# Performance work log

Hardware: AMD Instinct MI355X
Metric: run time of the kernel (lower is better)

Reference implementation:

```python
import jax, jax.numpy as jnp
import numpy as np
from jax import lax

B = 32768
N_INP = 256
N_HIDDEN = 1024
N_F = 256
N_ITERS = 100  # fixed-point solver iteration count in Convex


def _make_operators(n_f):
    # D = tridiag(-1, 2, -1) with first/last rows zeroed; mid = 0.5 * (sub+super diag ones)
    D = (-np.diag(np.ones(n_f - 1), -1) + 2 * np.diag(np.ones(n_f))
         - np.diag(np.ones(n_f - 1), 1)).astype(np.float32)
    D[0, :] = 0.0
    D[n_f - 1, :] = 0.0
    mid = 0.5 * (np.diag(np.ones(n_f - 1), -1) + np.diag(np.ones(n_f - 1), 1)).astype(np.float32)
    return jnp.asarray(D), jnp.asarray(mid)


def _convex(param):
    # param: [B, n_f]  (the torch code carries [B, n_f, 1]; column vec is equivalent)
    D, mid = _make_operators(param.shape[-1])

    def body(z, _):
        zx = z + param                       # [B, n_f]
        Dz = jnp.einsum('ij,bj->bi', D, zx)  # D @ zx
        mz = jnp.einsum('ij,bj->bi', mid, zx)
        dx = jnp.where(Dz > 0, zx - mz, 0.0)
        return zx - dx - param, None

    z0 = jnp.zeros_like(param)
    z_star, _ = lax.scan(body, z0, None, length=N_ITERS)
    return param + z_star  # Convex.forward: x + model(x)


def setup_inputs() -> dict:
    key = jax.random.key(0)
    k = jax.random.split(key, 5)
    x = jax.random.uniform(k[0], (B, N_INP + 1), dtype=jnp.float32)
    W1 = jax.random.normal(k[1], (N_HIDDEN, N_INP), dtype=jnp.float32) * 0.02
    b1 = jax.random.normal(k[2], (N_HIDDEN,), dtype=jnp.float32) * 0.02
    W2 = jax.random.normal(k[3], (N_F, N_HIDDEN), dtype=jnp.float32) * 0.02
    b2 = jax.random.normal(k[4], (N_F,), dtype=jnp.float32) * 0.02
    return {"x": x, "W1": W1, "b1": b1, "W2": W2, "b2": b2}


def reference(x, W1, b1, W2, b2):
    h = jax.nn.relu(x[..., :N_INP] @ W1.T + b1)     # [B, n_hidden]
    x_ = h @ W2.T + b2                              # [B, n_f]
    param = _convex(x_)                             # [B, n_f]
    # EvalConvex: round(query * (n_f - 1)) -> gather along feature dim
    idx = jnp.round(x[..., N_INP] * (N_F - 1)).astype(jnp.int32)  # [B]
    out = jnp.take_along_axis(param, idx[:, None], axis=1)        # [B, 1]
    return out.reshape(-1, 1, 1)                                  # [B, 1, 1]
```

## Files before the change

### kernel.cpp

```cpp
#include <hip/hip_runtime.h>
#include <stdint.h>

#define B_ROWS 32768
#define N_INP 256
#define N_HID 1024
#define NF 256
#define N_IT 100

typedef __attribute__((ext_vector_type(8))) _Float16 f16x8;
typedef __attribute__((ext_vector_type(4))) float f32x4;
typedef __attribute__((ext_vector_type(2))) _Float16 f16x2;
typedef uint32_t u32;

__device__ __forceinline__ ushort f2h(float f) {
  _Float16 h = (_Float16)f;
  return *reinterpret_cast<ushort*>(&h);
}

__device__ __forceinline__ void async_copy16(const void* g, void* l) {
  __builtin_amdgcn_global_load_lds(
      (const __attribute__((address_space(1))) void*)g,
      (__attribute__((address_space(3))) void*)l, 16, 0, 0);
}

__device__ __forceinline__ f16x2 as_h2(u32 x) { return __builtin_bit_cast(f16x2, x); }
__device__ __forceinline__ u32 as_u32(f16x2 x) { return __builtin_bit_cast(u32, x); }
__device__ __forceinline__ f16x2 min2(f16x2 a, f16x2 b) {
  f16x2 r;
  asm("v_pk_min_f16 %0, %1, %2" : "=v"(r) : "v"(a), "v"(b));
  return r;
}

__global__ void prep_kernel(const float* __restrict__ x,
                            const float* __restrict__ W1,
                            const float* __restrict__ W2,
                            ushort* __restrict__ xh,
                            ushort* __restrict__ w1h,
                            ushort* __restrict__ w2h,
                            int* __restrict__ idx) {
  if (blockIdx.x < 8192) {
    int t = blockIdx.x * 256 + threadIdx.x;
    int b = t >> 6, q = t & 63;
    const float* xr = x + (size_t)b * (N_INP + 1);
    float v0 = xr[q * 4 + 0], v1 = xr[q * 4 + 1], v2 = xr[q * 4 + 2], v3 = xr[q * 4 + 3];
    ushort4 u = make_ushort4(f2h(v0), f2h(v1), f2h(v2), f2h(v3));
    *reinterpret_cast<ushort4*>(xh + (size_t)b * 256 + q * 4) = u;
    if (q == 0) idx[b] = (int)rintf(xr[N_INP] * 255.0f);
  } else {
    int t = (blockIdx.x - 8192) * 256 + threadIdx.x;
    float4 a = reinterpret_cast<const float4*>(W1)[t];
    float4 b = reinterpret_cast<const float4*>(W2)[t];
    reinterpret_cast<ushort4*>(w1h)[t] = make_ushort4(f2h(a.x), f2h(a.y), f2h(a.z), f2h(a.w));
    reinterpret_cast<ushort4*>(w2h)[t] = make_ushort4(f2h(b.x), f2h(b.y), f2h(b.z), f2h(b.w));
  }
}

template <int RELU>
__global__ __launch_bounds__(256, 2) void gemm_bt(
    const ushort* __restrict__ A, const ushort* __restrict__ Bw,
    const float* __restrict__ bias, ushort* __restrict__ C,
    int M, int N, int K, int ntN) {
  __shared__ ushort As[2][128 * 64];
  __shared__ ushort Bs[2][128 * 64];
  const int tid = threadIdx.x;
  const int w = tid >> 6, l = tid & 63;
  int bid = blockIdx.x;
  if (((int)gridDim.x & 7) == 0) {
    int cpx = (int)gridDim.x >> 3;
    bid = (bid & 7) * cpx + (bid >> 3);
  }
  const int tm = bid / ntN, tn = bid % ntN;
  const int wm = w >> 1, wn = w & 1;
  const char* Ab = (const char*)(A + (size_t)tm * 128 * K);
  const char* Bb = (const char*)(Bw + (size_t)tn * 128 * K);
  const int sA = K * 2;
  const int lrow = l >> 3;
  const int lcol = (l & 7) * 16;

  f32x4 acc[4][4];
#pragma unroll
  for (int i = 0; i < 4; ++i)
#pragma unroll
    for (int j = 0; j < 4; ++j) acc[i][j] = {0.f, 0.f, 0.f, 0.f};

  const int nkt = K / 64;
  {
    const char* ga = Ab + lrow * sA + lcol;
    const char* gb = Bb + lrow * sA + lcol;
#pragma unroll
    for (int i = 0; i < 4; ++i) {
      int c = w * 4 + i;
      async_copy16(ga + c * 8 * sA, (char*)&As[0][0] + c * 1024);
      async_copy16(gb + c * 8 * sA, (char*)&Bs[0][0] + c * 1024);
    }
  }
  __syncthreads();

  const int arow = wm * 64 + (l & 15);
  const int brow = wn * 64 + (l & 15);
  const int koff = (l >> 4) * 8;

  for (int kt = 0; kt < nkt; ++kt) {
    const int buf = kt & 1;
    if (kt + 1 < nkt) {
      const char* ga = Ab + (kt + 1) * 128 + lrow * sA + lcol;
      const char* gb = Bb + (kt + 1) * 128 + lrow * sA + lcol;
#pragma unroll
      for (int i = 0; i < 4; ++i) {
        int c = w * 4 + i;
        async_copy16(ga + c * 8 * sA, (char*)&As[buf ^ 1][0] + c * 1024);
        async_copy16(gb + c * 8 * sA, (char*)&Bs[buf ^ 1][0] + c * 1024);
      }
    }
#pragma unroll
    for (int ks = 0; ks < 2; ++ks) {
      f16x8 af[4], bfr[4];
#pragma unroll
      for (int mi = 0; mi < 4; ++mi)
        af[mi] = *(const f16x8*)&As[buf][(arow + mi * 16) * 64 + ks * 32 + koff];
#pragma unroll
      for (int ni = 0; ni < 4; ++ni)
        bfr[ni] = *(const f16x8*)&Bs[buf][(brow + ni * 16) * 64 + ks * 32 + koff];
#pragma unroll
      for (int mi = 0; mi < 4; ++mi)
#pragma unroll
        for (int ni = 0; ni < 4; ++ni)
          acc[mi][ni] = __builtin_amdgcn_mfma_f32_16x16x32_f16(
              af[mi], bfr[ni], acc[mi][ni], 0, 0, 0);
    }
    __syncthreads();
  }

  const int grow0 = tm * 128 + wm * 64 + (l >> 4) * 4;
  const int gcol0 = tn * 128 + wn * 64 + (l & 15);
#pragma unroll
  for (int ni = 0; ni < 4; ++ni) {
    const int col = gcol0 + ni * 16;
    const float bv = bias[col];
#pragma unroll
    for (int mi = 0; mi < 4; ++mi) {
      const int row = grow0 + mi * 16;
#pragma unroll
      for (int r = 0; r < 4; ++r) {
        float v = acc[mi][ni][r] + bv;
        if (RELU) v = fmaxf(v, 0.f);
        C[(size_t)(row + r) * N + col] = f2h(v);
      }
    }
  }
}

__global__ __launch_bounds__(256) void convex_gather(
    const ushort* __restrict__ xqh, const int* __restrict__ idx,
    float* __restrict__ out) {
  const int l = threadIdx.x & 63;
  const int wv = threadIdx.x >> 6;
  const int q = l & 15;
  const int b = blockIdx.x * 16 + wv * 4 + (l >> 4);

  f16x2 h[8];
  {
    const uint4* src = reinterpret_cast<const uint4*>(xqh + (size_t)b * 256 + q * 16);
    uint4 v0 = src[0], v1 = src[1];
    h[0] = as_h2(v0.x); h[1] = as_h2(v0.y); h[2] = as_h2(v0.z); h[3] = as_h2(v0.w);
    h[4] = as_h2(v1.x); h[5] = as_h2(v1.y); h[6] = as_h2(v1.z); h[7] = as_h2(v1.w);
  }
  const int ii = idx[b];
  const int upIdx = ((l - 1) & 63) * 4;
  const int dnIdx = ((l + 1) & 63) * 4;
  const bool fixP = (q == 0);
  const bool fixN = (q == 15);
  const f16x2 halfc = {(_Float16)0.5f, (_Float16)0.5f};

  u32 P = __builtin_amdgcn_ds_bpermute(upIdx, as_u32(h[7]));
  u32 N = __builtin_amdgcn_ds_bpermute(dnIdx, as_u32(h[0]));

#pragma unroll 2
  for (int it = 0; it < N_IT; ++it) {
    u32 Pf = fixP ? 0x7C000000u : P;
    u32 Nf = fixN ? 0x00007C00u : N;
    f16x2 sm1 = as_h2(__builtin_amdgcn_alignbit(as_u32(h[0]), Pf, 16));
    f16x2 s0 = as_h2(__builtin_amdgcn_alignbit(as_u32(h[1]), as_u32(h[0]), 16));
    f16x2 s6 = as_h2(__builtin_amdgcn_alignbit(as_u32(h[7]), as_u32(h[6]), 16));
    f16x2 s7 = as_h2(__builtin_amdgcn_alignbit(Nf, as_u32(h[7]), 16));
    f16x2 s1 = as_h2(__builtin_amdgcn_alignbit(as_u32(h[2]), as_u32(h[1]), 16));
    f16x2 s2 = as_h2(__builtin_amdgcn_alignbit(as_u32(h[3]), as_u32(h[2]), 16));
    f16x2 s3 = as_h2(__builtin_amdgcn_alignbit(as_u32(h[4]), as_u32(h[3]), 16));
    f16x2 s4 = as_h2(__builtin_amdgcn_alignbit(as_u32(h[5]), as_u32(h[4]), 16));
    f16x2 s5 = as_h2(__builtin_amdgcn_alignbit(as_u32(h[6]), as_u32(h[5]), 16));
    h[0] = min2(h[0], (sm1 + s0) * halfc);
    h[7] = min2(h[7], (s6 + s7) * halfc);
    P = __builtin_amdgcn_ds_bpermute(upIdx, as_u32(h[7]));
    N = __builtin_amdgcn_ds_bpermute(dnIdx, as_u32(h[0]));
    h[1] = min2(h[1], (s0 + s1) * halfc);
    h[2] = min2(h[2], (s1 + s2) * halfc);
    h[3] = min2(h[3], (s2 + s3) * halfc);
    h[4] = min2(h[4], (s3 + s4) * halfc);
    h[5] = min2(h[5], (s4 + s5) * halfc);
    h[6] = min2(h[6], (s5 + s6) * halfc);
  }

  u32 r[8];
#pragma unroll
  for (int t = 0; t < 8; ++t) r[t] = as_u32(h[t]);
  const int sr = (ii >> 1) & 7;
#pragma unroll
  for (int step = 4; step >= 1; step >>= 1) {
#pragma unroll
    for (int k = 0; k < 4; ++k) {
      if (k < step) r[k] = (sr & step) ? r[k + step] : r[k];
    }
  }
  ushort hv = (ii & 1) ? (ushort)(r[0] >> 16) : (ushort)(r[0] & 0xffffu);
  float v = (float)__builtin_bit_cast(_Float16, hv);
  v = __shfl(v, (l & ~15) | (ii >> 4));
  if (q == 0) out[b] = v;
}

extern "C" void kernel_launch(void* const* d_in, const int* in_sizes, int n_in,
                              void* d_out, int out_size, void* d_ws, size_t ws_size,
                              hipStream_t stream) {
  const float* x = (const float*)d_in[0];
  const float* W1 = (const float*)d_in[1];
  const float* b1 = (const float*)d_in[2];
  const float* W2 = (const float*)d_in[3];
  const float* b2 = (const float*)d_in[4];
  float* out = (float*)d_out;

  char* ws = (char*)d_ws;
  ushort* xh  = (ushort*)ws;
  ushort* w1h = (ushort*)(ws + 16777216);
  ushort* w2h = (ushort*)(ws + 17301504);
  int*    idx = (int*)  (ws + 17825792);
  ushort* xqh = (ushort*)(ws + 17956864);
  ushort* h   = (ushort*)(ws + 34734080);

  const size_t fixed = 34734080;
  int chunk = 2048;
  if (ws_size >= fixed + (size_t)32768 * 2048) chunk = 32768;
  else if (ws_size >= fixed + (size_t)16384 * 2048) chunk = 16384;
  else if (ws_size >= fixed + (size_t)8192 * 2048) chunk = 8192;
  else if (ws_size >= fixed + (size_t)4096 * 2048) chunk = 4096;

  prep_kernel<<<8448, 256, 0, stream>>>(x, W1, W2, xh, w1h, w2h, idx);

  for (int m0 = 0; m0 < B_ROWS; m0 += chunk) {
    int curM = (B_ROWS - m0 < chunk) ? (B_ROWS - m0) : chunk;
    dim3 g1((curM / 128) * (N_HID / 128));
    gemm_bt<1><<<g1, 256, 0, stream>>>(xh + (size_t)m0 * 256, w1h, b1, h,
                                       curM, N_HID, N_INP, N_HID / 128);
    dim3 g2((curM / 128) * (NF / 128));
    gemm_bt<0><<<g2, 256, 0, stream>>>(h, w2h, b2, xqh + (size_t)m0 * 256,
                                       curM, NF, N_HID, NF / 128);
  }
  convex_gather<<<B_ROWS / 16, 256, 0, stream>>>(xqh, idx, out);
}
```

Before: 133.7 us.

## Give each thread 64 features per row, 4 lanes per row in convex solver

The convex fixed-point kernel now assigns 4 lanes per row, each holding 64 fp16 values in 32 packed registers, instead of 16 lanes holding 16 values. This cuts the share of cross-lane bpermute traffic and boundary handling per useful update, and each block covers four times as many rows. The cost is much higher register pressure per thread and a serial dependency chain of 32 packed updates per iteration. The final gather uses a deeper select tree and a narrower shuffle.

```diff
diff --git a/kernel.cpp b/kernel.cpp
--- a/kernel.cpp
+++ b/kernel.cpp
@@ -153,68 +153,64 @@
 __global__ __launch_bounds__(256) void convex_gather(
     const ushort* __restrict__ xqh, const int* __restrict__ idx,
     float* __restrict__ out) {
-  const int l = threadIdx.x & 63;
-  const int wv = threadIdx.x >> 6;
-  const int q = l & 15;
-  const int b = blockIdx.x * 16 + wv * 4 + (l >> 4);
-
-  f16x2 h[8];
+  const int tid = threadIdx.x;
+  const int l = tid & 63;
+  const int w = tid >> 6;
+  const int q = l & 3;
+  const int row = blockIdx.x * 64 + w * 16 + (l >> 2);
+
+  u32 y[32];
   {
-    const uint4* src = reinterpret_cast<const uint4*>(xqh + (size_t)b * 256 + q * 16);
-    uint4 v0 = src[0], v1 = src[1];
-    h[0] = as_h2(v0.x); h[1] = as_h2(v0.y); h[2] = as_h2(v0.z); h[3] = as_h2(v0.w);
-    h[4] = as_h2(v1.x); h[5] = as_h2(v1.y); h[6] = as_h2(v1.z); h[7] = as_h2(v1.w);
-  }
-  const int ii = idx[b];
+    const uint4* src = reinterpret_cast<const uint4*>(xqh + (size_t)row * 256 + q * 64);
+#pragma unroll
+    for (int j = 0; j < 8; ++j) {
+      uint4 v = src[j];
+      y[j * 4 + 0] = v.x; y[j * 4 + 1] = v.y; y[j * 4 + 2] = v.z; y[j * 4 + 3] = v.w;
+    }
+  }
+  const int ii = idx[row];
   const int upIdx = ((l - 1) & 63) * 4;
   const int dnIdx = ((l + 1) & 63) * 4;
   const bool fixP = (q == 0);
-  const bool fixN = (q == 15);
+  const bool fixN = (q == 3);
   const f16x2 halfc = {(_Float16)0.5f, (_Float16)0.5f};
 
-  u32 P = __builtin_amdgcn_ds_bpermute(upIdx, as_u32(h[7]));
-  u32 N = __builtin_amdgcn_ds_bpermute(dnIdx, as_u32(h[0]));
-
-#pragma unroll 2
+  u32 P = __builtin_amdgcn_ds_bpermute(upIdx, y[31]);
+  u32 N = __builtin_amdgcn_ds_bpermute(dnIdx, y[0]);
+
   for (int it = 0; it < N_IT; ++it) {
-    u32 Pf = fixP ? 0x7C000000u : P;
-    u32 Nf = fixN ? 0x00007C00u : N;
-    f16x2 sm1 = as_h2(__builtin_amdgcn_alignbit(as_u32(h[0]), Pf, 16));
-    f16x2 s0 = as_h2(__builtin_amdgcn_alignbit(as_u32(h[1]), as_u32(h[0]), 16));
-    f16x2 s6 = as_h2(__builtin_amdgcn_alignbit(as_u32(h[7]), as_u32(h[6]), 16));
-    f16x2 s7 = as_h2(__builtin_amdgcn_alignbit(Nf, as_u32(h[7]), 16));
-    f16x2 s1 = as_h2(__builtin_amdgcn_alignbit(as_u32(h[2]), as_u32(h[1]), 16));
-    f16x2 s2 = as_h2(__builtin_amdgcn_alignbit(as_u32(h[3]), as_u32(h[2]), 16));
-    f16x2 s3 = as_h2(__builtin_amdgcn_alignbit(as_u32(h[4]), as_u32(h[3]), 16));
-    f16x2 s4 = as_h2(__builtin_amdgcn_alignbit(as_u32(h[5]), as_u32(h[4]), 16));
-    f16x2 s5 = as_h2(__builtin_amdgcn_alignbit(as_u32(h[6]), as_u32(h[5]), 16));
-    h[0] = min2(h[0], (sm1 + s0) * halfc);
-    h[7] = min2(h[7], (s6 + s7) * halfc);
-    P = __builtin_amdgcn_ds_bpermute(upIdx, as_u32(h[7]));
-    N = __builtin_amdgcn_ds_bpermute(dnIdx, as_u32(h[0]));
-    h[1] = min2(h[1], (s0 + s1) * halfc);
-    h[2] = min2(h[2], (s1 + s2) * halfc);
-    h[3] = min2(h[3], (s2 + s3) * halfc);
-    h[4] = min2(h[4], (s3 + s4) * halfc);
-    h[5] = min2(h[5], (s4 + s5) * halfc);
-    h[6] = min2(h[6], (s5 + s6) * halfc);
-  }
-
-  u32 r[8];
-#pragma unroll
-  for (int t = 0; t < 8; ++t) r[t] = as_u32(h[t]);
-  const int sr = (ii >> 1) & 7;
-#pragma unroll
-  for (int step = 4; step >= 1; step >>= 1) {
-#pragma unroll
-    for (int k = 0; k < 4; ++k) {
-      if (k < step) r[k] = (sr & step) ? r[k + step] : r[k];
-    }
-  }
-  ushort hv = (ii & 1) ? (ushort)(r[0] >> 16) : (ushort)(r[0] & 0xffffu);
+    const u32 Pf = fixP ? 0x7C000000u : P;
+    const u32 Nf = fixN ? 0x00007C00u : N;
+    f16x2 s31 = as_h2(__builtin_amdgcn_alignbit(y[31], y[30], 16));
+    f16x2 s32 = as_h2(__builtin_amdgcn_alignbit(Nf, y[31], 16));
+    f16x2 s0 = as_h2(__builtin_amdgcn_alignbit(y[0], Pf, 16));
+    f16x2 s1 = as_h2(__builtin_amdgcn_alignbit(y[1], y[0], 16));
+    y[31] = as_u32(min2(as_h2(y[31]), (s31 + s32) * halfc));
+    y[0] = as_u32(min2(as_h2(y[0]), (s0 + s1) * halfc));
+    P = __builtin_amdgcn_ds_bpermute(upIdx, y[31]);
+    N = __builtin_amdgcn_ds_bpermute(dnIdx, y[0]);
+    f16x2 sp = s1;
+#pragma unroll
+    for (int t = 1; t < 31; ++t) {
+      f16x2 sn = (t == 30) ? s31
+                           : as_h2(__builtin_amdgcn_alignbit(y[t + 1], y[t], 16));
+      y[t] = as_u32(min2(as_h2(y[t]), (sp + sn) * halfc));
+      sp = sn;
+    }
+  }
+
+  const int sel = (ii >> 1) & 31;
+#pragma unroll
+  for (int step = 16; step >= 1; step >>= 1) {
+#pragma unroll
+    for (int k = 0; k < 16; ++k) {
+      if (k < step) y[k] = (sel & step) ? y[k + step] : y[k];
+    }
+  }
+  ushort hv = (ii & 1) ? (ushort)(y[0] >> 16) : (ushort)(y[0] & 0xffffu);
   float v = (float)__builtin_bit_cast(_Float16, hv);
-  v = __shfl(v, (l & ~15) | (ii >> 4));
-  if (q == 0) out[b] = v;
+  v = __shfl(v, (l & ~3) | (ii >> 6));
+  if (q == 0) out[row] = v;
 }
 
 extern "C" void kernel_launch(void* const* d_in, const int* in_sizes, int n_in,
@@ -253,5 +249,5 @@
     gemm_bt<0><<<g2, 256, 0, stream>>>(h, w2h, b2, xqh + (size_t)m0 * 256,
                                        curM, NF, N_HID, NF / 128);
   }
-  convex_gather<<<B_ROWS / 16, 256, 0, stream>>>(xqh, idx, out);
-}
+  convex_gather<<<B_ROWS / 64, 256, 0, stream>>>(xqh, idx, out);
+}
```

After: 145.0 us. 8.4% more time.
